# Performance work log

Measured on AMD Instinct MI355X. Metric: run time of the kernel, lower is better.

## Reference

```python
import jax, jax.numpy as jnp
import numpy as np

B, T, C = 2, 4096, 768
H = 12
D = C // H  # head_dim = 64


def setup_inputs() -> dict:
    key = jax.random.key(0)
    kx, kq, kk, kv, ko = jax.random.split(key, 5)
    s = 1.0 / np.sqrt(C)  # keep activations well-scaled
    return {
        "x": jax.random.normal(kx, (B, T, C), dtype=jnp.float32),
        "wq": jax.random.normal(kq, (C, C), dtype=jnp.float32) * s,
        "wk": jax.random.normal(kk, (C, C), dtype=jnp.float32) * s,
        "wv": jax.random.normal(kv, (C, C), dtype=jnp.float32) * s,
        "wo": jax.random.normal(ko, (C, C), dtype=jnp.float32) * s,
    }


def reference(x, wq, wk, wv, wo):
    b, t, c = x.shape
    # projections (torch Linear: y = x @ W.T); split heads -> (B,H,T,D)
    q = (x @ wq.T).reshape(b, t, H, D).transpose(0, 2, 1, 3)
    k = (x @ wk.T).reshape(b, t, H, D).transpose(0, 2, 1, 3)
    v = (x @ wv.T).reshape(b, t, H, D).transpose(0, 2, 1, 3)
    scale = 1.0 / jnp.sqrt(jnp.asarray(D, dtype=x.dtype))
    scores = jnp.einsum("bhqd,bhkd->bhqk", q, k) * scale  # (B,H,T,T)
    causal = jnp.tril(jnp.ones((t, t), dtype=bool))
    scores = jnp.where(causal, scores, jnp.asarray(-jnp.inf, dtype=scores.dtype))
    attn = jax.nn.softmax(scores, axis=-1)
    ctx = jnp.einsum("bhqk,bhkd->bhqd", attn, v)  # (B,H,T,D)
    ctx = ctx.transpose(0, 2, 1, 3).reshape(b, t, c)
    return ctx @ wo.T
```

## Files before the change

### kernel.cpp

```cpp
#include <hip/hip_runtime.h>
#include <hip/hip_bf16.h>

#define B_  2
#define T_  4096
#define C_  768
#define H_  12
#define D_  64
#define MTOT (B_*T_)

typedef __bf16 bf16;
typedef __bf16 bf16x8 __attribute__((ext_vector_type(8)));
typedef __bf16 bf16x4 __attribute__((ext_vector_type(4)));
typedef float  f32x4  __attribute__((ext_vector_type(4)));

__device__ __forceinline__ void gl_lds16(const bf16* g, bf16* l) {
    __builtin_amdgcn_global_load_lds(
        (const __attribute__((address_space(1))) void*)g,
        (__attribute__((address_space(3))) void*)l, 16, 0, 0);
}

__global__ __launch_bounds__(256) void cvt_bf16(const float* __restrict__ src,
                                                bf16* __restrict__ dst, int n8) {
    int i = blockIdx.x * 256 + threadIdx.x;
    if (i >= n8) return;
    const float4* s4 = (const float4*)src;
    float4 a = s4[2*(size_t)i], b = s4[2*(size_t)i+1];
    bf16x8 o;
    o[0]=(bf16)a.x; o[1]=(bf16)a.y; o[2]=(bf16)a.z; o[3]=(bf16)a.w;
    o[4]=(bf16)b.x; o[5]=(bf16)b.y; o[6]=(bf16)b.z; o[7]=(bf16)b.w;
    *(bf16x8*)(dst + 8*(size_t)i) = o;
}

__global__ __launch_bounds__(256) void cvt_bf16_w4(const float* __restrict__ w0,
                                                   const float* __restrict__ w1,
                                                   const float* __restrict__ w2,
                                                   const float* __restrict__ w3,
                                                   bf16* __restrict__ d0,
                                                   bf16* __restrict__ d1,
                                                   bf16* __restrict__ d2,
                                                   bf16* __restrict__ d3) {
    int z = blockIdx.y;
    const float* src = (z==0)?w0:(z==1)?w1:(z==2)?w2:w3;
    bf16* dst = (z==0)?d0:(z==1)?d1:(z==2)?d2:d3;
    int i = blockIdx.x * 256 + threadIdx.x;
    const float4* s4 = (const float4*)src;
    float4 a = s4[2*(size_t)i], b = s4[2*(size_t)i+1];
    bf16x8 o;
    o[0]=(bf16)a.x; o[1]=(bf16)a.y; o[2]=(bf16)a.z; o[3]=(bf16)a.w;
    o[4]=(bf16)b.x; o[5]=(bf16)b.y; o[6]=(bf16)b.z; o[7]=(bf16)b.w;
    *(bf16x8*)(dst + 8*(size_t)i) = o;
}

__global__ __launch_bounds__(256) void gemm_qkv(const bf16* __restrict__ xb,
                                                const bf16* __restrict__ wqb,
                                                const bf16* __restrict__ wkb,
                                                const bf16* __restrict__ wvb,
                                                bf16* __restrict__ qo,
                                                bf16* __restrict__ ko,
                                                bf16* __restrict__ vto) {
    int z = blockIdx.z;
    const bf16* w = (z == 0) ? wqb : (z == 1) ? wkb : wvb;
    bf16* dst = (z == 0) ? qo : (z == 1) ? ko : vto;
    int mbase = blockIdx.x * 128;
    int nbase = blockIdx.y * 128;
    __shared__ bf16 As[128][32];
    __shared__ bf16 Bs[128][32];
    int tid  = threadIdx.x;
    int wave = tid >> 6, lane = tid & 63;
    int wm = (wave >> 1) * 64, wn = (wave & 1) * 64;
    int lr = lane & 15, lg = lane >> 4;
    int srow0 = tid >> 2, scol0 = tid & 3;
    int srow1 = (tid + 256) >> 2, scol1 = (tid + 256) & 3;
    f32x4 acc[4][4] = {};
    for (int kb = 0; kb < C_; kb += 32) {
        gl_lds16(xb + (size_t)(mbase + srow0) * C_ + kb + scol0 * 8, &As[srow0][scol0 * 8]);
        gl_lds16(xb + (size_t)(mbase + srow1) * C_ + kb + scol1 * 8, &As[srow1][scol1 * 8]);
        gl_lds16(w  + (size_t)(nbase + srow0) * C_ + kb + scol0 * 8, &Bs[srow0][scol0 * 8]);
        gl_lds16(w  + (size_t)(nbase + srow1) * C_ + kb + scol1 * 8, &Bs[srow1][scol1 * 8]);
        __syncthreads();
        bf16x8 af[4], bfr[4];
        #pragma unroll
        for (int mt = 0; mt < 4; ++mt) af[mt]  = *(const bf16x8*)(&As[wm + mt*16 + lr][lg*8]);
        #pragma unroll
        for (int nt = 0; nt < 4; ++nt) bfr[nt] = *(const bf16x8*)(&Bs[wn + nt*16 + lr][lg*8]);
        #pragma unroll
        for (int mt = 0; mt < 4; ++mt)
            #pragma unroll
            for (int nt = 0; nt < 4; ++nt)
                acc[mt][nt] = __builtin_amdgcn_mfma_f32_16x16x32_bf16(af[mt], bfr[nt], acc[mt][nt], 0, 0, 0);
        __syncthreads();
    }
    float sc = (z == 0) ? 0.18033688011112042f : 1.0f;
    int m0 = mbase + wm + (lg << 2);
    int n0 = nbase + wn + lr;
    if (z < 2) {
        #pragma unroll
        for (int mt = 0; mt < 4; ++mt) {
            #pragma unroll
            for (int nt = 0; nt < 4; ++nt) {
                int n = n0 + nt * 16;
                int h = n >> 6, d = n & 63;
                #pragma unroll
                for (int r = 0; r < 4; ++r) {
                    int m = m0 + mt * 16 + r;
                    int b = m >> 12, t = m & 4095;
                    dst[(((size_t)b * H_ + h) * T_ + t) * 64 + d] = (bf16)(acc[mt][nt][r] * sc);
                }
            }
        }
    } else {
        #pragma unroll
        for (int mt = 0; mt < 4; ++mt) {
            int m = m0 + mt * 16;
            int b = m >> 12, t = m & 4095;
            #pragma unroll
            for (int nt = 0; nt < 4; ++nt) {
                int n = n0 + nt * 16;
                int h = n >> 6, d = n & 63;
                bf16x4 pk;
                #pragma unroll
                for (int r = 0; r < 4; ++r) pk[r] = (bf16)acc[mt][nt][r];
                *(bf16x4*)(dst + (((size_t)b * H_ + h) * 64 + d) * T_ + t) = pk;
            }
        }
    }
}

__global__ __launch_bounds__(256) void gemm_out(const bf16* __restrict__ ctx,
                                                const bf16* __restrict__ wob,
                                                float* __restrict__ out) {
    int mbase = blockIdx.x * 128;
    int nbase = blockIdx.y * 128;
    __shared__ bf16 As[128][32];
    __shared__ bf16 Bs[128][32];
    int tid  = threadIdx.x;
    int wave = tid >> 6, lane = tid & 63;
    int wm = (wave >> 1) * 64, wn = (wave & 1) * 64;
    int lr = lane & 15, lg = lane >> 4;
    int srow0 = tid >> 2, scol0 = tid & 3;
    int srow1 = (tid + 256) >> 2, scol1 = (tid + 256) & 3;
    f32x4 acc[4][4] = {};
    for (int kb = 0; kb < C_; kb += 32) {
        gl_lds16(ctx + (size_t)(mbase + srow0) * C_ + kb + scol0 * 8, &As[srow0][scol0 * 8]);
        gl_lds16(ctx + (size_t)(mbase + srow1) * C_ + kb + scol1 * 8, &As[srow1][scol1 * 8]);
        gl_lds16(wob + (size_t)(nbase + srow0) * C_ + kb + scol0 * 8, &Bs[srow0][scol0 * 8]);
        gl_lds16(wob + (size_t)(nbase + srow1) * C_ + kb + scol1 * 8, &Bs[srow1][scol1 * 8]);
        __syncthreads();
        bf16x8 af[4], bfr[4];
        #pragma unroll
        for (int mt = 0; mt < 4; ++mt) af[mt]  = *(const bf16x8*)(&As[wm + mt*16 + lr][lg*8]);
        #pragma unroll
        for (int nt = 0; nt < 4; ++nt) bfr[nt] = *(const bf16x8*)(&Bs[wn + nt*16 + lr][lg*8]);
        #pragma unroll
        for (int mt = 0; mt < 4; ++mt)
            #pragma unroll
            for (int nt = 0; nt < 4; ++nt)
                acc[mt][nt] = __builtin_amdgcn_mfma_f32_16x16x32_bf16(af[mt], bfr[nt], acc[mt][nt], 0, 0, 0);
        __syncthreads();
    }
    int m0 = mbase + wm + (lg << 2);
    int n0 = nbase + wn + lr;
    #pragma unroll
    for (int mt = 0; mt < 4; ++mt)
        #pragma unroll
        for (int nt = 0; nt < 4; ++nt)
            #pragma unroll
            for (int r = 0; r < 4; ++r)
                out[(size_t)(m0 + mt * 16 + r) * C_ + n0 + nt * 16] = acc[mt][nt][r];
}

__global__ __launch_bounds__(256, 4) void attn(const bf16* __restrict__ q,
                                               const bf16* __restrict__ k,
                                               const bf16* __restrict__ vt,
                                               bf16* __restrict__ ctx) {
    int idx = blockIdx.x;
    int qt = 63 - idx / 24;
    int bh = idx % 24;
    int b = bh / H_, h = bh % H_;
    int tid = threadIdx.x;
    int wave = tid >> 6, lane = tid & 63;
    int lr = lane & 15, lg = lane >> 4;

    __shared__ bf16 Ks[64][72];
    __shared__ bf16 Vs[64][72];
    __shared__ bf16 Pb[4][16][72];

    const bf16* qp = q  + (size_t)bh * T_ * 64;
    const bf16* kp = k  + (size_t)bh * T_ * 64;
    const bf16* vp = vt + (size_t)bh * 64 * (size_t)T_;

    int r0 = tid >> 3, c0 = tid & 7;
    const bf16* kstg = kp + (size_t)r0 * 64 + c0 * 8;
    const bf16* vstg = vp + (size_t)r0 * T_ + c0 * 8;

    const float NEGINF = -__builtin_inff();

    int qb = qt * 64 + wave * 16;
    int n  = qt + 1;
    int qrow = qb + lr;

    bf16x8 qf[2];
    #pragma unroll
    for (int c = 0; c < 2; ++c)
        qf[c] = *(const bf16x8*)(qp + (size_t)(qb + lr) * 64 + c * 32 + lg * 8);

    f32x4 o[4] = {};
    float m = NEGINF, l = 0.f;

    uint4 sk0 = *(const uint4*)(kstg);
    uint4 sk1 = *(const uint4*)(kstg + 32 * 64);
    uint4 sv0 = *(const uint4*)(vstg);
    uint4 sv1 = *(const uint4*)(vstg + (size_t)32 * T_);

    for (int kb = 0; kb < n; ++kb) {
        int kv = kb * 64;
        __syncthreads();
        *(uint4*)(&Ks[r0][c0 * 8])      = sk0;
        *(uint4*)(&Ks[32 + r0][c0 * 8]) = sk1;
        *(uint4*)(&Vs[r0][c0 * 8])      = sv0;
        *(uint4*)(&Vs[32 + r0][c0 * 8]) = sv1;
        if (kb + 1 < n) {
            const bf16* ksrc = kstg + (size_t)(kb + 1) * 64 * 64;
            const bf16* vsrc = vstg + (size_t)(kb + 1) * 64;
            sk0 = *(const uint4*)(ksrc);
            sk1 = *(const uint4*)(ksrc + 32 * 64);
            sv0 = *(const uint4*)(vsrc);
            sv1 = *(const uint4*)(vsrc + (size_t)32 * T_);
        }
        __syncthreads();

        f32x4 s[4] = {};
        #pragma unroll
        for (int c2 = 0; c2 < 2; ++c2)
            #pragma unroll
            for (int nt = 0; nt < 4; ++nt) {
                bf16x8 kf = *(const bf16x8*)(&Ks[nt * 16 + lr][c2 * 32 + lg * 8]);
                s[nt] = __builtin_amdgcn_mfma_f32_16x16x32_bf16(kf, qf[c2], s[nt], 0, 0, 0);
            }
        if (kb == qt) {
            #pragma unroll
            for (int nt = 0; nt < 4; ++nt)
                #pragma unroll
                for (int r = 0; r < 4; ++r) {
                    int key = kv + nt * 16 + lg * 4 + r;
                    s[nt][r] = (key > qrow) ? NEGINF : s[nt][r];
                }
        }
        float mx = s[0][0];
        #pragma unroll
        for (int nt = 0; nt < 4; ++nt) {
            float a = fmaxf(s[nt][0], s[nt][1]);
            float bq = fmaxf(s[nt][2], s[nt][3]);
            mx = fmaxf(mx, fmaxf(a, bq));
        }
        mx = fmaxf(mx, __shfl_xor(mx, 16, 64));
        mx = fmaxf(mx, __shfl_xor(mx, 32, 64));
        float mn = fmaxf(m, mx);
        float al = __builtin_amdgcn_exp2f(m - mn);
        m = mn;
        float sm = 0.f;
        #pragma unroll
        for (int nt = 0; nt < 4; ++nt)
            #pragma unroll
            for (int r = 0; r < 4; ++r) {
                float p = __builtin_amdgcn_exp2f(s[nt][r] - mn);
                s[nt][r] = p;
                sm += p;
            }
        sm += __shfl_xor(sm, 16, 64);
        sm += __shfl_xor(sm, 32, 64);
        l = l * al + sm;
        #pragma unroll
        for (int dt = 0; dt < 4; ++dt)
            #pragma unroll
            for (int r = 0; r < 4; ++r) o[dt][r] *= al;
        #pragma unroll
        for (int nt = 0; nt < 4; ++nt) {
            bf16x4 pk;
            #pragma unroll
            for (int r = 0; r < 4; ++r) pk[r] = (bf16)s[nt][r];
            *(bf16x4*)(&Pb[wave][lr][nt * 16 + lg * 4]) = pk;
        }
        #pragma unroll
        for (int c2 = 0; c2 < 2; ++c2) {
            bf16x8 pf = *(const bf16x8*)(&Pb[wave][lr][c2 * 32 + lg * 8]);
            #pragma unroll
            for (int dt = 0; dt < 4; ++dt) {
                bf16x8 vfr = *(const bf16x8*)(&Vs[dt * 16 + lr][c2 * 32 + lg * 8]);
                o[dt] = __builtin_amdgcn_mfma_f32_16x16x32_bf16(vfr, pf, o[dt], 0, 0, 0);
            }
        }
    }

    float inv = 1.0f / l;
    #pragma unroll
    for (int dt = 0; dt < 4; ++dt) {
        bf16x4 pk;
        #pragma unroll
        for (int r = 0; r < 4; ++r) pk[r] = (bf16)(o[dt][r] * inv);
        *(bf16x4*)(ctx + ((size_t)b * T_ + qb + lr) * C_ + h * 64 + dt * 16 + lg * 4) = pk;
    }
}

extern "C" void kernel_launch(void* const* d_in, const int* in_sizes, int n_in,
                              void* d_out, int out_size, void* d_ws, size_t ws_size,
                              hipStream_t stream) {
    const float* x  = (const float*)d_in[0];
    const float* wq = (const float*)d_in[1];
    const float* wk = (const float*)d_in[2];
    const float* wv = (const float*)d_in[3];
    const float* wo = (const float*)d_in[4];
    float* out = (float*)d_out;

    char* ws = (char*)d_ws;
    const size_t SZ_XB = (size_t)MTOT * C_ * sizeof(bf16);
    const size_t SZ_W  = (size_t)C_ * C_ * sizeof(bf16);
    bf16* xb  = (bf16*)(ws);
    bf16* wqb = (bf16*)(ws + SZ_XB);
    bf16* wkb = (bf16*)(ws + SZ_XB + SZ_W);
    bf16* wvb = (bf16*)(ws + SZ_XB + 2 * SZ_W);
    bf16* wob = (bf16*)(ws + SZ_XB + 3 * SZ_W);
    bf16* qb  = (bf16*)(ws + SZ_XB + 4 * SZ_W);
    bf16* kb  = (bf16*)(ws + 2 * SZ_XB + 4 * SZ_W);
    bf16* vtb = (bf16*)(ws + 3 * SZ_XB + 4 * SZ_W);
    bf16* ctb = (bf16*)(ws + 4 * SZ_XB + 4 * SZ_W);

    cvt_bf16<<<3072, 256, 0, stream>>>(x, xb, MTOT * C_ / 8);
    cvt_bf16_w4<<<dim3(288, 4), 256, 0, stream>>>(wq, wk, wv, wo, wqb, wkb, wvb, wob);

    gemm_qkv<<<dim3(MTOT / 128, C_ / 128, 3), 256, 0, stream>>>(xb, wqb, wkb, wvb, qb, kb, vtb);
    attn<<<1536, 256, 0, stream>>>(qb, kb, vtb, ctb);
    gemm_out<<<dim3(MTOT / 128, C_ / 128), 256, 0, stream>>>(ctb, wob, out);
}
```

Before: 249.7 us.

## Pair low and high causal query tiles per block and add lazy softmax rescale

Each attention block now handles two query tiles, a low one and its mirror high one, so every block does the same amount of causal work. The two tiles share each staged K/V tile, which halves the grid and reuses the shared-memory loads. The softmax also skips rescaling the running max unless it grows by more than a threshold, and MFMA sections get raised wave priority. The cost is more registers (launch bounds drop to 3 blocks), fewer blocks (768) to cover the CUs, and more shared memory for a second P buffer.

New measurement: 250.7 us. About the same (+0.4%).

```diff
diff --git a/kernel.cpp b/kernel.cpp
--- a/kernel.cpp
+++ b/kernel.cpp
@@ -169,13 +169,68 @@
                 out[(size_t)(m0 + mt * 16 + r) * C_ + n0 + nt * 16] = acc[mt][nt][r];
 }
 
-__global__ __launch_bounds__(256, 4) void attn(const bf16* __restrict__ q,
+__device__ __forceinline__ void softmax_tile(f32x4 (&s)[4], float& m, float& l, f32x4 (&o)[4],
+                                             bf16 (*pb)[72], int lr, int lg) {
+    float mx = fmaxf(fmaxf(s[0][0], s[0][1]), fmaxf(s[0][2], s[0][3]));
+    #pragma unroll
+    for (int nt = 1; nt < 4; ++nt) {
+        float a = fmaxf(s[nt][0], s[nt][1]);
+        float bq = fmaxf(s[nt][2], s[nt][3]);
+        mx = fmaxf(mx, fmaxf(a, bq));
+    }
+    mx = fmaxf(mx, __shfl_xor(mx, 16, 64));
+    mx = fmaxf(mx, __shfl_xor(mx, 32, 64));
+    if (!__all(mx <= m + 8.0f)) {
+        float mn = fmaxf(m, mx);
+        float al = __builtin_amdgcn_exp2f(m - mn);
+        m = mn;
+        l *= al;
+        #pragma unroll
+        for (int dt = 0; dt < 4; ++dt)
+            #pragma unroll
+            for (int r = 0; r < 4; ++r) o[dt][r] *= al;
+    }
+    float sm = 0.f;
+    #pragma unroll
+    for (int nt = 0; nt < 4; ++nt)
+        #pragma unroll
+        for (int r = 0; r < 4; ++r) {
+            float p = __builtin_amdgcn_exp2f(s[nt][r] - m);
+            s[nt][r] = p;
+            sm += p;
+        }
+    sm += __shfl_xor(sm, 16, 64);
+    sm += __shfl_xor(sm, 32, 64);
+    l += sm;
+    #pragma unroll
+    for (int nt = 0; nt < 4; ++nt) {
+        bf16x4 pk;
+        #pragma unroll
+        for (int r = 0; r < 4; ++r) pk[r] = (bf16)s[nt][r];
+        *(bf16x4*)(&pb[lr][nt * 16 + lg * 4]) = pk;
+    }
+}
+
+__device__ __forceinline__ void attn_store(const f32x4 (&o)[4], float l, bf16* __restrict__ ctx,
+                                           int b, int qrow, int h, int lg) {
+    float inv = 1.0f / l;
+    #pragma unroll
+    for (int dt = 0; dt < 4; ++dt) {
+        bf16x4 pk;
+        #pragma unroll
+        for (int r = 0; r < 4; ++r) pk[r] = (bf16)(o[dt][r] * inv);
+        *(bf16x4*)(ctx + ((size_t)b * T_ + qrow) * C_ + h * 64 + dt * 16 + lg * 4) = pk;
+    }
+}
+
+__global__ __launch_bounds__(256, 3) void attn(const bf16* __restrict__ q,
                                                const bf16* __restrict__ k,
                                                const bf16* __restrict__ vt,
                                                bf16* __restrict__ ctx) {
     int idx = blockIdx.x;
-    int qt = 63 - idx / 24;
-    int bh = idx % 24;
+    int qlo = idx / 24;
+    int qhi = 63 - qlo;
+    int bh  = idx % 24;
     int b = bh / H_, h = bh % H_;
     int tid = threadIdx.x;
     int wave = tid >> 6, lane = tid & 63;
@@ -183,7 +238,8 @@
 
     __shared__ bf16 Ks[64][72];
     __shared__ bf16 Vs[64][72];
-    __shared__ bf16 Pb[4][16][72];
+    __shared__ bf16 PbA[4][16][72];
+    __shared__ bf16 PbB[4][16][72];
 
     const bf16* qp = q  + (size_t)bh * T_ * 64;
     const bf16* kp = k  + (size_t)bh * T_ * 64;
@@ -195,31 +251,36 @@
 
     const float NEGINF = -__builtin_inff();
 
-    int qb = qt * 64 + wave * 16;
-    int n  = qt + 1;
-    int qrow = qb + lr;
-
-    bf16x8 qf[2];
-    #pragma unroll
-    for (int c = 0; c < 2; ++c)
-        qf[c] = *(const bf16x8*)(qp + (size_t)(qb + lr) * 64 + c * 32 + lg * 8);
-
-    f32x4 o[4] = {};
-    float m = NEGINF, l = 0.f;
+    int qbA = qlo * 64 + wave * 16;
+    int qbB = qhi * 64 + wave * 16;
+    int qrowA = qbA + lr, qrowB = qbB + lr;
+    int nkb = qhi + 1;
+
+    bf16x8 qfA[2], qfB[2];
+    #pragma unroll
+    for (int c = 0; c < 2; ++c) {
+        qfA[c] = *(const bf16x8*)(qp + (size_t)(qbA + lr) * 64 + c * 32 + lg * 8);
+        qfB[c] = *(const bf16x8*)(qp + (size_t)(qbB + lr) * 64 + c * 32 + lg * 8);
+    }
+
+    f32x4 oA[4] = {}, oB[4] = {};
+    float mA = NEGINF, lA = 0.f;
+    float mB = NEGINF, lB = 0.f;
 
     uint4 sk0 = *(const uint4*)(kstg);
     uint4 sk1 = *(const uint4*)(kstg + 32 * 64);
     uint4 sv0 = *(const uint4*)(vstg);
     uint4 sv1 = *(const uint4*)(vstg + (size_t)32 * T_);
 
-    for (int kb = 0; kb < n; ++kb) {
+    for (int kb = 0; kb < nkb; ++kb) {
         int kv = kb * 64;
+        bool paired = (kb <= qlo);
         __syncthreads();
         *(uint4*)(&Ks[r0][c0 * 8])      = sk0;
         *(uint4*)(&Ks[32 + r0][c0 * 8]) = sk1;
         *(uint4*)(&Vs[r0][c0 * 8])      = sv0;
         *(uint4*)(&Vs[32 + r0][c0 * 8]) = sv1;
-        if (kb + 1 < n) {
+        if (kb + 1 < nkb) {
             const bf16* ksrc = kstg + (size_t)(kb + 1) * 64 * 64;
             const bf16* vsrc = vstg + (size_t)(kb + 1) * 64;
             sk0 = *(const uint4*)(ksrc);
@@ -229,77 +290,79 @@
         }
         __syncthreads();
 
-        f32x4 s[4] = {};
-        #pragma unroll
-        for (int c2 = 0; c2 < 2; ++c2)
-            #pragma unroll
-            for (int nt = 0; nt < 4; ++nt) {
-                bf16x8 kf = *(const bf16x8*)(&Ks[nt * 16 + lr][c2 * 32 + lg * 8]);
-                s[nt] = __builtin_amdgcn_mfma_f32_16x16x32_bf16(kf, qf[c2], s[nt], 0, 0, 0);
-            }
-        if (kb == qt) {
-            #pragma unroll
-            for (int nt = 0; nt < 4; ++nt)
-                #pragma unroll
-                for (int r = 0; r < 4; ++r) {
-                    int key = kv + nt * 16 + lg * 4 + r;
-                    s[nt][r] = (key > qrow) ? NEGINF : s[nt][r];
-                }
-        }
-        float mx = s[0][0];
-        #pragma unroll
-        for (int nt = 0; nt < 4; ++nt) {
-            float a = fmaxf(s[nt][0], s[nt][1]);
-            float bq = fmaxf(s[nt][2], s[nt][3]);
-            mx = fmaxf(mx, fmaxf(a, bq));
-        }
-        mx = fmaxf(mx, __shfl_xor(mx, 16, 64));
-        mx = fmaxf(mx, __shfl_xor(mx, 32, 64));
-        float mn = fmaxf(m, mx);
-        float al = __builtin_amdgcn_exp2f(m - mn);
-        m = mn;
-        float sm = 0.f;
-        #pragma unroll
-        for (int nt = 0; nt < 4; ++nt)
-            #pragma unroll
-            for (int r = 0; r < 4; ++r) {
-                float p = __builtin_amdgcn_exp2f(s[nt][r] - mn);
-                s[nt][r] = p;
-                sm += p;
-            }
-        sm += __shfl_xor(sm, 16, 64);
-        sm += __shfl_xor(sm, 32, 64);
-        l = l * al + sm;
-        #pragma unroll
-        for (int dt = 0; dt < 4; ++dt)
-            #pragma unroll
-            for (int r = 0; r < 4; ++r) o[dt][r] *= al;
-        #pragma unroll
-        for (int nt = 0; nt < 4; ++nt) {
-            bf16x4 pk;
-            #pragma unroll
-            for (int r = 0; r < 4; ++r) pk[r] = (bf16)s[nt][r];
-            *(bf16x4*)(&Pb[wave][lr][nt * 16 + lg * 4]) = pk;
-        }
-        #pragma unroll
-        for (int c2 = 0; c2 < 2; ++c2) {
-            bf16x8 pf = *(const bf16x8*)(&Pb[wave][lr][c2 * 32 + lg * 8]);
-            #pragma unroll
-            for (int dt = 0; dt < 4; ++dt) {
-                bf16x8 vfr = *(const bf16x8*)(&Vs[dt * 16 + lr][c2 * 32 + lg * 8]);
-                o[dt] = __builtin_amdgcn_mfma_f32_16x16x32_bf16(vfr, pf, o[dt], 0, 0, 0);
-            }
-        }
-    }
-
-    float inv = 1.0f / l;
-    #pragma unroll
-    for (int dt = 0; dt < 4; ++dt) {
-        bf16x4 pk;
-        #pragma unroll
-        for (int r = 0; r < 4; ++r) pk[r] = (bf16)(o[dt][r] * inv);
-        *(bf16x4*)(ctx + ((size_t)b * T_ + qb + lr) * C_ + h * 64 + dt * 16 + lg * 4) = pk;
-    }
+        if (paired) {
+            f32x4 sA[4] = {}, sB[4] = {};
+            __builtin_amdgcn_s_setprio(1);
+            #pragma unroll
+            for (int c2 = 0; c2 < 2; ++c2)
+                #pragma unroll
+                for (int nt = 0; nt < 4; ++nt) {
+                    bf16x8 kf = *(const bf16x8*)(&Ks[nt * 16 + lr][c2 * 32 + lg * 8]);
+                    sB[nt] = __builtin_amdgcn_mfma_f32_16x16x32_bf16(kf, qfB[c2], sB[nt], 0, 0, 0);
+                    sA[nt] = __builtin_amdgcn_mfma_f32_16x16x32_bf16(kf, qfA[c2], sA[nt], 0, 0, 0);
+                }
+            __builtin_amdgcn_s_setprio(0);
+            if (kb == qlo) {
+                #pragma unroll
+                for (int nt = 0; nt < 4; ++nt)
+                    #pragma unroll
+                    for (int r = 0; r < 4; ++r) {
+                        int key = kv + nt * 16 + lg * 4 + r;
+                        sA[nt][r] = (key > qrowA) ? NEGINF : sA[nt][r];
+                    }
+            }
+            softmax_tile(sB, mB, lB, oB, PbB[wave], lr, lg);
+            softmax_tile(sA, mA, lA, oA, PbA[wave], lr, lg);
+            __builtin_amdgcn_s_setprio(1);
+            #pragma unroll
+            for (int c2 = 0; c2 < 2; ++c2) {
+                bf16x8 pfB = *(const bf16x8*)(&PbB[wave][lr][c2 * 32 + lg * 8]);
+                bf16x8 pfA = *(const bf16x8*)(&PbA[wave][lr][c2 * 32 + lg * 8]);
+                #pragma unroll
+                for (int dt = 0; dt < 4; ++dt) {
+                    bf16x8 vfr = *(const bf16x8*)(&Vs[dt * 16 + lr][c2 * 32 + lg * 8]);
+                    oB[dt] = __builtin_amdgcn_mfma_f32_16x16x32_bf16(vfr, pfB, oB[dt], 0, 0, 0);
+                    oA[dt] = __builtin_amdgcn_mfma_f32_16x16x32_bf16(vfr, pfA, oA[dt], 0, 0, 0);
+                }
+            }
+            __builtin_amdgcn_s_setprio(0);
+        } else {
+            f32x4 sB[4] = {};
+            __builtin_amdgcn_s_setprio(1);
+            #pragma unroll
+            for (int c2 = 0; c2 < 2; ++c2)
+                #pragma unroll
+                for (int nt = 0; nt < 4; ++nt) {
+                    bf16x8 kf = *(const bf16x8*)(&Ks[nt * 16 + lr][c2 * 32 + lg * 8]);
+                    sB[nt] = __builtin_amdgcn_mfma_f32_16x16x32_bf16(kf, qfB[c2], sB[nt], 0, 0, 0);
+                }
+            __builtin_amdgcn_s_setprio(0);
+            if (kb == qhi) {
+                #pragma unroll
+                for (int nt = 0; nt < 4; ++nt)
+                    #pragma unroll
+                    for (int r = 0; r < 4; ++r) {
+                        int key = kv + nt * 16 + lg * 4 + r;
+                        sB[nt][r] = (key > qrowB) ? NEGINF : sB[nt][r];
+                    }
+            }
+            softmax_tile(sB, mB, lB, oB, PbB[wave], lr, lg);
+            __builtin_amdgcn_s_setprio(1);
+            #pragma unroll
+            for (int c2 = 0; c2 < 2; ++c2) {
+                bf16x8 pfB = *(const bf16x8*)(&PbB[wave][lr][c2 * 32 + lg * 8]);
+                #pragma unroll
+                for (int dt = 0; dt < 4; ++dt) {
+                    bf16x8 vfr = *(const bf16x8*)(&Vs[dt * 16 + lr][c2 * 32 + lg * 8]);
+                    oB[dt] = __builtin_amdgcn_mfma_f32_16x16x32_bf16(vfr, pfB, oB[dt], 0, 0, 0);
+                }
+            }
+            __builtin_amdgcn_s_setprio(0);
+        }
+    }
+
+    attn_store(oA, lA, ctx, b, qrowA, h, lg);
+    attn_store(oB, lB, ctx, b, qrowB, h, lg);
 }
 
 extern "C" void kernel_launch(void* const* d_in, const int* in_sizes, int n_in,
@@ -329,6 +392,6 @@
     cvt_bf16_w4<<<dim3(288, 4), 256, 0, stream>>>(wq, wk, wv, wo, wqb, wkb, wvb, wob);
 
     gemm_qkv<<<dim3(MTOT / 128, C_ / 128, 3), 256, 0, stream>>>(xb, wqb, wkb, wvb, qb, kb, vtb);
-    attn<<<1536, 256, 0, stream>>>(qb, kb, vtb, ctb);
+    attn<<<768, 256, 0, stream>>>(qb, kb, vtb, ctb);
     gemm_out<<<dim3(MTOT / 128, C_ / 128), 256, 0, stream>>>(ctb, wob, out);
 }
```

## Transpose P in registers via permlane swaps, add lazy rescaling and setprio in attention

Applied to the files above, without the earlier changes.

Drops the per-wave LDS staging buffer for P. The softmax probabilities are packed with v_cvt_pk_bf16_f32 and redistributed into the MFMA B-operand layout using permlane32/permlane16 swaps, which removes an LDS write/read round trip and frees shared memory. It also skips the rescaling of o and l unless the running max grows by more than 8 (lazy rescale), brackets the MFMA sections with s_setprio, and raises the launch-bounds occupancy hint from 4 to 6. The risks are register pressure at the higher occupancy target and an incorrect lane mapping in the permlane transpose.

Result: slower. 259.2 us (+3.8%).

```diff
diff --git a/kernel.cpp b/kernel.cpp
--- a/kernel.cpp
+++ b/kernel.cpp
@@ -12,11 +12,23 @@
 typedef __bf16 bf16x8 __attribute__((ext_vector_type(8)));
 typedef __bf16 bf16x4 __attribute__((ext_vector_type(4)));
 typedef float  f32x4  __attribute__((ext_vector_type(4)));
+typedef unsigned int u32x4 __attribute__((ext_vector_type(4)));
 
 __device__ __forceinline__ void gl_lds16(const bf16* g, bf16* l) {
     __builtin_amdgcn_global_load_lds(
         (const __attribute__((address_space(1))) void*)g,
         (__attribute__((address_space(3))) void*)l, 16, 0, 0);
+}
+
+__device__ __forceinline__ void pswap32_16(unsigned int& x, unsigned int& y) {
+    auto r1 = __builtin_amdgcn_permlane32_swap(x, y, false, false);
+    auto r2 = __builtin_amdgcn_permlane16_swap(r1[0], r1[1], false, false);
+    x = r2[0]; y = r2[1];
+}
+__device__ __forceinline__ unsigned int cvtpk(float lo, float hi) {
+    unsigned int r;
+    asm("v_cvt_pk_bf16_f32 %0, %1, %2" : "=v"(r) : "v"(lo), "v"(hi));
+    return r;
 }
 
 __global__ __launch_bounds__(256) void cvt_bf16(const float* __restrict__ src,
@@ -169,7 +181,19 @@
                 out[(size_t)(m0 + mt * 16 + r) * C_ + n0 + nt * 16] = acc[mt][nt][r];
 }
 
-__global__ __launch_bounds__(256, 4) void attn(const bf16* __restrict__ q,
+__device__ __forceinline__ void attn_store(const f32x4 (&o)[4], float l, bf16* __restrict__ ctx,
+                                           int b, int qrow, int h, int lg) {
+    float inv = 1.0f / l;
+    #pragma unroll
+    for (int dt = 0; dt < 4; ++dt) {
+        bf16x4 pk;
+        #pragma unroll
+        for (int r = 0; r < 4; ++r) pk[r] = (bf16)(o[dt][r] * inv);
+        *(bf16x4*)(ctx + ((size_t)b * T_ + qrow) * C_ + h * 64 + dt * 16 + lg * 4) = pk;
+    }
+}
+
+__global__ __launch_bounds__(256, 6) void attn(const bf16* __restrict__ q,
                                                const bf16* __restrict__ k,
                                                const bf16* __restrict__ vt,
                                                bf16* __restrict__ ctx) {
@@ -183,7 +207,6 @@
 
     __shared__ bf16 Ks[64][72];
     __shared__ bf16 Vs[64][72];
-    __shared__ bf16 Pb[4][16][72];
 
     const bf16* qp = q  + (size_t)bh * T_ * 64;
     const bf16* kp = k  + (size_t)bh * T_ * 64;
@@ -230,6 +253,7 @@
         __syncthreads();
 
         f32x4 s[4] = {};
+        __builtin_amdgcn_s_setprio(1);
         #pragma unroll
         for (int c2 = 0; c2 < 2; ++c2)
             #pragma unroll
@@ -237,6 +261,7 @@
                 bf16x8 kf = *(const bf16x8*)(&Ks[nt * 16 + lr][c2 * 32 + lg * 8]);
                 s[nt] = __builtin_amdgcn_mfma_f32_16x16x32_bf16(kf, qf[c2], s[nt], 0, 0, 0);
             }
+        __builtin_amdgcn_s_setprio(0);
         if (kb == qt) {
             #pragma unroll
             for (int nt = 0; nt < 4; ++nt)
@@ -246,60 +271,69 @@
                     s[nt][r] = (key > qrow) ? NEGINF : s[nt][r];
                 }
         }
-        float mx = s[0][0];
-        #pragma unroll
-        for (int nt = 0; nt < 4; ++nt) {
+        float mx = fmaxf(fmaxf(s[0][0], s[0][1]), fmaxf(s[0][2], s[0][3]));
+        #pragma unroll
+        for (int nt = 1; nt < 4; ++nt) {
             float a = fmaxf(s[nt][0], s[nt][1]);
             float bq = fmaxf(s[nt][2], s[nt][3]);
             mx = fmaxf(mx, fmaxf(a, bq));
         }
         mx = fmaxf(mx, __shfl_xor(mx, 16, 64));
         mx = fmaxf(mx, __shfl_xor(mx, 32, 64));
-        float mn = fmaxf(m, mx);
-        float al = __builtin_amdgcn_exp2f(m - mn);
-        m = mn;
+        if (!__all(mx <= m + 8.0f)) {
+            float mn = fmaxf(m, mx);
+            float al = __builtin_amdgcn_exp2f(m - mn);
+            m = mn;
+            l *= al;
+            #pragma unroll
+            for (int dt = 0; dt < 4; ++dt)
+                #pragma unroll
+                for (int r = 0; r < 4; ++r) o[dt][r] *= al;
+        }
         float sm = 0.f;
         #pragma unroll
         for (int nt = 0; nt < 4; ++nt)
             #pragma unroll
             for (int r = 0; r < 4; ++r) {
-                float p = __builtin_amdgcn_exp2f(s[nt][r] - mn);
+                float p = __builtin_amdgcn_exp2f(s[nt][r] - m);
                 s[nt][r] = p;
                 sm += p;
             }
         sm += __shfl_xor(sm, 16, 64);
         sm += __shfl_xor(sm, 32, 64);
-        l = l * al + sm;
-        #pragma unroll
-        for (int dt = 0; dt < 4; ++dt)
-            #pragma unroll
-            for (int r = 0; r < 4; ++r) o[dt][r] *= al;
+        l += sm;
+        unsigned int dpk[8];
         #pragma unroll
         for (int nt = 0; nt < 4; ++nt) {
-            bf16x4 pk;
-            #pragma unroll
-            for (int r = 0; r < 4; ++r) pk[r] = (bf16)s[nt][r];
-            *(bf16x4*)(&Pb[wave][lr][nt * 16 + lg * 4]) = pk;
-        }
+            dpk[2*nt]   = cvtpk(s[nt][0], s[nt][1]);
+            dpk[2*nt+1] = cvtpk(s[nt][2], s[nt][3]);
+        }
+        unsigned int pw[2][4];
+        #pragma unroll
+        for (int c2 = 0; c2 < 2; ++c2)
+            #pragma unroll
+            for (int pr = 0; pr < 2; ++pr) {
+                unsigned int x = dpk[4*c2 + pr], y = dpk[4*c2 + 2 + pr];
+                pswap32_16(x, y);
+                pw[c2][pr] = x;
+                pw[c2][2+pr] = y;
+            }
+        __builtin_amdgcn_s_setprio(1);
         #pragma unroll
         for (int c2 = 0; c2 < 2; ++c2) {
-            bf16x8 pf = *(const bf16x8*)(&Pb[wave][lr][c2 * 32 + lg * 8]);
+            u32x4 pt;
+            pt[0] = pw[c2][0]; pt[1] = pw[c2][1]; pt[2] = pw[c2][2]; pt[3] = pw[c2][3];
+            bf16x8 pf = __builtin_bit_cast(bf16x8, pt);
             #pragma unroll
             for (int dt = 0; dt < 4; ++dt) {
                 bf16x8 vfr = *(const bf16x8*)(&Vs[dt * 16 + lr][c2 * 32 + lg * 8]);
                 o[dt] = __builtin_amdgcn_mfma_f32_16x16x32_bf16(vfr, pf, o[dt], 0, 0, 0);
             }
         }
-    }
-
-    float inv = 1.0f / l;
-    #pragma unroll
-    for (int dt = 0; dt < 4; ++dt) {
-        bf16x4 pk;
-        #pragma unroll
-        for (int r = 0; r < 4; ++r) pk[r] = (bf16)(o[dt][r] * inv);
-        *(bf16x4*)(ctx + ((size_t)b * T_ + qb + lr) * C_ + h * 64 + dt * 16 + lg * 4) = pk;
-    }
+        __builtin_amdgcn_s_setprio(0);
+    }
+
+    attn_store(o, l, ctx, b, qrow, h, lg);
 }
 
 extern "C" void kernel_launch(void* const* d_in, const int* in_sizes, int n_in,
```
